# Performance work log

Measured on AMD Instinct MI355X. Metric: run time of the kernel, lower is better.

## Reference

```python
import jax, jax.numpy as jnp
import numpy as np

N_NODES = 50000
N_EDGES = 800000
N_FEAT = 256
HIDDEN = 128
N_CLASSES = 40


def gcn_conv(x, src, dst, W, b, n_nodes):
    """PyG GCNConv: add self-loops, symmetric normalization, x@W then scatter-add."""
    h = x @ W  # [N, out]
    loop = jnp.arange(n_nodes, dtype=src.dtype)
    s = jnp.concatenate([src, loop])  # [E+N]
    d = jnp.concatenate([dst, loop])
    deg = jax.ops.segment_sum(jnp.ones_like(d, dtype=h.dtype), d, num_segments=n_nodes)
    dinv = jnp.where(deg > 0, jax.lax.rsqrt(deg), 0.0)
    norm = dinv[s] * dinv[d]  # [E+N]
    msg = h[s] * norm[:, None]  # gather + scale
    out = jax.ops.segment_sum(msg, d, num_segments=n_nodes)  # scatter-add to targets
    return out + b


def setup_inputs() -> dict:
    key = jax.random.key(0)
    k1, k2, k3, k4 = jax.random.split(key, 4)
    x = jax.random.normal(k1, (N_NODES, N_FEAT), dtype=jnp.float32)
    edge_index = jax.random.randint(k2, (2, N_EDGES), 0, N_NODES, dtype=jnp.int32)
    # Glorot-style init for conv weights, zero bias (PyG default)
    W1 = jax.random.normal(k3, (N_FEAT, HIDDEN), dtype=jnp.float32) * (1.0 / np.sqrt(N_FEAT))
    b1 = jnp.zeros((HIDDEN,), dtype=jnp.float32)
    W2 = jax.random.normal(k4, (HIDDEN, N_CLASSES), dtype=jnp.float32) * (1.0 / np.sqrt(HIDDEN))
    b2 = jnp.zeros((N_CLASSES,), dtype=jnp.float32)
    return {"x": x, "edge_index": edge_index, "W1": W1, "b1": b1, "W2": W2, "b2": b2}


def reference(x, edge_index, W1, b1, W2, b2):
    # eval mode: dropout is identity
    src, dst = edge_index[0], edge_index[1]
    h = gcn_conv(x, src, dst, W1, b1, N_NODES)
    h = jax.nn.relu(h)
    h = gcn_conv(h, src, dst, W2, b2, N_NODES)
    return jax.nn.log_softmax(h, axis=1)
```

## Files before the change

### kernel.cpp

```cpp
#include <hip/hip_runtime.h>
#include <cstdint>

#define N_NODES 50000
#define N_EDGES 800000
#define N_FEAT 256
#define HIDDEN 128
#define N_CLASSES 40
#define NBUCKET 196
#define EPB 3125
#define BCAP 8192
#define ROWS_PAD 50048
#define H2S 64

typedef __attribute__((ext_vector_type(8))) short bf16x8;
typedef __attribute__((ext_vector_type(4))) float f32x4;

__device__ inline ushort f2bf(float f) {
    union { float f; uint u; } v; v.f = f;
    uint u = v.u;
    u += 0x7fff + ((u >> 16) & 1);
    return (ushort)(u >> 16);
}
__device__ inline float bflo(uint u) {
    union { uint u; float f; } v; v.u = u << 16; return v.f;
}
__device__ inline float bfhi(uint u) {
    union { uint u; float f; } v; v.u = u & 0xffff0000u; return v.f;
}


__global__ __launch_bounds__(256) void partition_repack(
        const int* __restrict__ src, const int* __restrict__ dst,
        int* __restrict__ cursor, uint* __restrict__ ebuf,
        const float* __restrict__ W1, ushort* __restrict__ Bp1) {
    __shared__ int h[NBUCKET];
    __shared__ int base[NBUCKET];
    __shared__ int cur[NBUCKET];
    int blk = blockIdx.x, t = threadIdx.x;
    int gid = blk * 256 + t;
    if (gid < 32768) {
        int j = gid & 7, lane = (gid >> 3) & 63, kt = (gid >> 9) & 7, nt = gid >> 12;
        int k = kt * 32 + (lane >> 4) * 8 + j;
        int n = nt * 16 + (lane & 15);
        Bp1[gid] = f2bf(W1[k * HIDDEN + n]);
    }
    if (t < NBUCKET) { h[t] = 0; cur[t] = 0; }
    __syncthreads();
    int eb = blk * EPB;
    for (int i = t; i < EPB; i += 256)
        atomicAdd(&h[dst[eb + i] >> 8], 1);
    __syncthreads();
    if (t < NBUCKET)
        base[t] = (h[t] > 0) ? atomicAdd(&cursor[t], h[t]) : 0;
    __syncthreads();
    for (int i = t; i < EPB; i += 256) {
        int d = dst[eb + i], sv = src[eb + i];
        int bk = d >> 8;
        int p = base[bk] + atomicAdd(&cur[bk], 1);
        ebuf[bk * BCAP + p] = ((uint)d << 16) | (uint)sv;
    }
}


__global__ __launch_bounds__(256) void bucket_csr(
        const uint* __restrict__ ebuf, const int* __restrict__ cursor,
        int* __restrict__ deg, float* __restrict__ dinv,
        int* __restrict__ rowptr, int* __restrict__ esrc) {
    __shared__ int s[256];
    __shared__ int cnt[256];
    __shared__ int exc[256];
    __shared__ int cur[256];
    int b = blockIdx.x, t = threadIdx.x;
    s[t] = (t < NBUCKET) ? cursor[t] : 0;
    __syncthreads();
    for (int off = 1; off < 256; off <<= 1) {
        int t2 = 0;
        if (t >= off) t2 = s[t - off];
        __syncthreads();
        s[t] += t2;
        __syncthreads();
    }
    int beg = (b > 0) ? s[b - 1] : 0;
    int ecnt = s[b] - beg;
    __syncthreads();
    cnt[t] = 0;
    cur[t] = 0;
    __syncthreads();
    const uint* eb = ebuf + (size_t)b * BCAP;
    for (int i = t; i < ecnt; i += 256)
        atomicAdd(&cnt[(eb[i] >> 16) & 255], 1);
    __syncthreads();
    int d = cnt[t];
    s[t] = d;
    __syncthreads();
    for (int off = 1; off < 256; off <<= 1) {
        int t2 = 0;
        if (t >= off) t2 = s[t - off];
        __syncthreads();
        s[t] += t2;
        __syncthreads();
    }
    exc[t] = s[t] - d;
    int node = b * 256 + t;
    if (node < N_NODES) {
        deg[node] = d;
        dinv[node] = rsqrtf((float)(d + 1));
        rowptr[node] = beg + exc[t];
    }
    __syncthreads();
    for (int i = t; i < ecnt; i += 256) {
        uint u = eb[i];
        int dl = (int)(u >> 16) & 255;
        int pos = beg + exc[dl] + atomicAdd(&cur[dl], 1);
        esrc[pos] = (int)(u & 0xffffu);
    }
}


#define XS_STRIDE 264

__global__ __launch_bounds__(256) void gemm1_mfma(const float* __restrict__ x,
                                                  const ushort* __restrict__ Bp,
                                                  ushort* __restrict__ h1b) {
    __shared__ ushort xs[64 * XS_STRIDE];
    int t = threadIdx.x;
    int row0 = blockIdx.x * 64;
#pragma unroll
    for (int i = 0; i < 16; ++i) {
        int idx = t + i * 256;
        int r = idx >> 6, kg = idx & 63;
        int row = row0 + r;
        float4 v = make_float4(0.f, 0.f, 0.f, 0.f);
        if (row < N_NODES) v = *(const float4*)(x + (size_t)row * N_FEAT + kg * 4);
        ushort4 u;
        u.x = f2bf(v.x); u.y = f2bf(v.y); u.z = f2bf(v.z); u.w = f2bf(v.w);
        *(ushort4*)(&xs[r * XS_STRIDE + kg * 4]) = u;
    }
    __syncthreads();
    int lane = t & 63, w = t >> 6;
    int r = lane & 15, q = lane >> 4;
    f32x4 acc[8] = {};
    for (int kt = 0; kt < 8; ++kt) {
        bf16x8 a = *(const bf16x8*)(&xs[(w * 16 + r) * XS_STRIDE + kt * 32 + q * 8]);
#pragma unroll
        for (int nt = 0; nt < 8; ++nt) {
            bf16x8 b = *(const bf16x8*)(Bp + (((nt * 8 + kt) * 64) + lane) * 8);
            acc[nt] = __builtin_amdgcn_mfma_f32_16x16x32_bf16(a, b, acc[nt], 0, 0, 0);
        }
    }
#pragma unroll
    for (int nt = 0; nt < 8; ++nt) {
        int col = nt * 16 + r;
#pragma unroll
        for (int reg = 0; reg < 4; ++reg) {
            int row = row0 + w * 16 + q * 4 + reg;
            if (row < N_NODES) h1b[(size_t)row * HIDDEN + col] = f2bf(acc[nt][reg]);
        }
    }
}


__global__ __launch_bounds__(256) void agg1_g(
        const int* __restrict__ rowptr, const int* __restrict__ deg,
        const int* __restrict__ esrc, const float* __restrict__ dinv,
        const ushort* __restrict__ h1b, const float* __restrict__ b1,
        ushort* __restrict__ hagb) {
    int w = threadIdx.x >> 6, lane = threadIdx.x & 63;
    int v = blockIdx.x * 4 + w;
    int q = lane >> 4, l = lane & 15;
    int beg = rowptr[v], d = deg[v];
    float dv = dinv[v];
    float a0 = 0.f, a1 = 0.f, a2 = 0.f, a3 = 0.f;
    float a4 = 0.f, a5 = 0.f, a6 = 0.f, a7 = 0.f;
    if (q == 0) {
        uint4 hv = *(const uint4*)(h1b + (size_t)v * HIDDEN + l * 8);
        float dd = dv * dv;
        a0 = bflo(hv.x) * dd; a1 = bfhi(hv.x) * dd;
        a2 = bflo(hv.y) * dd; a3 = bfhi(hv.y) * dd;
        a4 = bflo(hv.z) * dd; a5 = bfhi(hv.z) * dd;
        a6 = bflo(hv.w) * dd; a7 = bfhi(hv.w) * dd;
    }
    int e_l = (lane < d) ? esrc[beg + lane] : 0;
    float w_l = (lane < d) ? dinv[e_l] : 0.f;
    int dm = min(d, 64);
    int i = 0;
    for (; i + 8 <= dm; i += 8) {
        int s0 = __shfl(e_l, i + q, 64);
        int s1 = __shfl(e_l, i + 4 + q, 64);
        float g0 = __shfl(w_l, i + q, 64) * dv;
        float g1 = __shfl(w_l, i + 4 + q, 64) * dv;
        uint4 h0 = *(const uint4*)(h1b + (size_t)s0 * HIDDEN + l * 8);
        uint4 h1 = *(const uint4*)(h1b + (size_t)s1 * HIDDEN + l * 8);
        a0 = fmaf(bflo(h0.x), g0, a0); a1 = fmaf(bfhi(h0.x), g0, a1);
        a2 = fmaf(bflo(h0.y), g0, a2); a3 = fmaf(bfhi(h0.y), g0, a3);
        a4 = fmaf(bflo(h0.z), g0, a4); a5 = fmaf(bfhi(h0.z), g0, a5);
        a6 = fmaf(bflo(h0.w), g0, a6); a7 = fmaf(bfhi(h0.w), g0, a7);
        a0 = fmaf(bflo(h1.x), g1, a0); a1 = fmaf(bfhi(h1.x), g1, a1);
        a2 = fmaf(bflo(h1.y), g1, a2); a3 = fmaf(bfhi(h1.y), g1, a3);
        a4 = fmaf(bflo(h1.z), g1, a4); a5 = fmaf(bfhi(h1.z), g1, a5);
        a6 = fmaf(bflo(h1.w), g1, a6); a7 = fmaf(bfhi(h1.w), g1, a7);
    }
    for (; i < dm; i += 4) {
        int idx = i + q;
        int cl = idx & 63;
        int s0 = __shfl(e_l, cl, 64);
        float g0 = __shfl(w_l, cl, 64) * dv;
        if (idx >= dm) g0 = 0.f;
        uint4 h0 = *(const uint4*)(h1b + (size_t)s0 * HIDDEN + l * 8);
        a0 = fmaf(bflo(h0.x), g0, a0); a1 = fmaf(bfhi(h0.x), g0, a1);
        a2 = fmaf(bflo(h0.y), g0, a2); a3 = fmaf(bfhi(h0.y), g0, a3);
        a4 = fmaf(bflo(h0.z), g0, a4); a5 = fmaf(bfhi(h0.z), g0, a5);
        a6 = fmaf(bflo(h0.w), g0, a6); a7 = fmaf(bfhi(h0.w), g0, a7);
    }
    for (int j = 64 + q; j < d; j += 4) {
        int s = esrc[beg + j];
        float g = dinv[s] * dv;
        uint4 hs = *(const uint4*)(h1b + (size_t)s * HIDDEN + l * 8);
        a0 = fmaf(bflo(hs.x), g, a0); a1 = fmaf(bfhi(hs.x), g, a1);
        a2 = fmaf(bflo(hs.y), g, a2); a3 = fmaf(bfhi(hs.y), g, a3);
        a4 = fmaf(bflo(hs.z), g, a4); a5 = fmaf(bfhi(hs.z), g, a5);
        a6 = fmaf(bflo(hs.w), g, a6); a7 = fmaf(bfhi(hs.w), g, a7);
    }
    a0 += __shfl_xor(a0, 16, 64); a0 += __shfl_xor(a0, 32, 64);
    a1 += __shfl_xor(a1, 16, 64); a1 += __shfl_xor(a1, 32, 64);
    a2 += __shfl_xor(a2, 16, 64); a2 += __shfl_xor(a2, 32, 64);
    a3 += __shfl_xor(a3, 16, 64); a3 += __shfl_xor(a3, 32, 64);
    a4 += __shfl_xor(a4, 16, 64); a4 += __shfl_xor(a4, 32, 64);
    a5 += __shfl_xor(a5, 16, 64); a5 += __shfl_xor(a5, 32, 64);
    a6 += __shfl_xor(a6, 16, 64); a6 += __shfl_xor(a6, 32, 64);
    a7 += __shfl_xor(a7, 16, 64); a7 += __shfl_xor(a7, 32, 64);
    if (q == 0) {
        float4 bb0 = ((const float4*)b1)[l * 2];
        float4 bb1 = ((const float4*)b1)[l * 2 + 1];
        a0 += bb0.x; a1 += bb0.y; a2 += bb0.z; a3 += bb0.w;
        a4 += bb1.x; a5 += bb1.y; a6 += bb1.z; a7 += bb1.w;
        a0 = a0 > 0.f ? a0 : 0.f;  a1 = a1 > 0.f ? a1 : 0.f;
        a2 = a2 > 0.f ? a2 : 0.f;  a3 = a3 > 0.f ? a3 : 0.f;
        a4 = a4 > 0.f ? a4 : 0.f;  a5 = a5 > 0.f ? a5 : 0.f;
        a6 = a6 > 0.f ? a6 : 0.f;  a7 = a7 > 0.f ? a7 : 0.f;
        uint4 o;
        o.x = ((uint)f2bf(a1) << 16) | (uint)f2bf(a0);
        o.y = ((uint)f2bf(a3) << 16) | (uint)f2bf(a2);
        o.z = ((uint)f2bf(a5) << 16) | (uint)f2bf(a4);
        o.w = ((uint)f2bf(a7) << 16) | (uint)f2bf(a6);
        *(uint4*)(hagb + (size_t)v * HIDDEN + l * 8) = o;
    }
}


__global__ void repack_W2(const float* __restrict__ W, ushort* __restrict__ Bp) {
    int idx = blockIdx.x * 256 + threadIdx.x;
    if (idx >= 6144) return;
    int j = idx & 7, lane = (idx >> 3) & 63, kt = (idx >> 9) & 3, nt = idx >> 11;
    int k = kt * 32 + (lane >> 4) * 8 + j;
    int n = nt * 16 + (lane & 15);
    Bp[idx] = (n < N_CLASSES) ? f2bf(W[k * N_CLASSES + n]) : (ushort)0;
}

__global__ __launch_bounds__(256) void gemm2_mfma(const ushort* __restrict__ hagb,
                                                  const ushort* __restrict__ Bp,
                                                  ushort* __restrict__ h2b) {
    int t = threadIdx.x;
    int lane = t & 63, w = t >> 6;
    int r = lane & 15, q = lane >> 4;
    int row0 = blockIdx.x * 64;
    int arow = row0 + w * 16 + r;
    f32x4 acc[3] = {};
    for (int kt = 0; kt < 4; ++kt) {
        bf16x8 a = *(const bf16x8*)(hagb + (size_t)arow * HIDDEN + kt * 32 + q * 8);
#pragma unroll
        for (int nt = 0; nt < 3; ++nt) {
            bf16x8 b = *(const bf16x8*)(Bp + (((nt * 4 + kt) * 64) + lane) * 8);
            acc[nt] = __builtin_amdgcn_mfma_f32_16x16x32_bf16(a, b, acc[nt], 0, 0, 0);
        }
    }
#pragma unroll
    for (int nt = 0; nt < 3; ++nt) {
        int col = nt * 16 + r;
        if (col >= N_CLASSES) continue;
#pragma unroll
        for (int reg = 0; reg < 4; ++reg) {
            int row = row0 + w * 16 + q * 4 + reg;
            if (row < N_NODES) h2b[(size_t)row * H2S + col] = f2bf(acc[nt][reg]);
        }
    }
}


__global__ __launch_bounds__(256) void agg2_lsm(
        const int* __restrict__ rowptr, const int* __restrict__ deg,
        const int* __restrict__ esrc, const float* __restrict__ dinv,
        const ushort* __restrict__ h2b, const float* __restrict__ b2,
        float* __restrict__ out) {
    int w = threadIdx.x >> 6, lane = threadIdx.x & 63;
    int v = blockIdx.x * 4 + w;
    int g3 = lane / 20;
    int l = lane - g3 * 20;
    bool act = g3 < 3;
    int beg = rowptr[v], d = deg[v];
    float dv = dinv[v];
    float ax = 0.f, ay = 0.f;
    if (lane < 20) {
        uint hv = *(const uint*)(h2b + (size_t)v * H2S + l * 2);
        ax = bflo(hv) * dv * dv;
        ay = bfhi(hv) * dv * dv;
    }
    int e_l = (lane < d) ? esrc[beg + lane] : 0;
    float w_l = (lane < d) ? dinv[e_l] : 0.f;
    int dm = min(d, 64);
    int i = 0;
    for (; i + 6 <= dm; i += 6) {
        int s0 = __shfl(e_l, (i + g3) & 63, 64);
        int s1 = __shfl(e_l, (i + 3 + g3) & 63, 64);
        float g0 = __shfl(w_l, (i + g3) & 63, 64) * dv;
        float g1 = __shfl(w_l, (i + 3 + g3) & 63, 64) * dv;
        if (!act) { g0 = 0.f; g1 = 0.f; }
        uint h0 = *(const uint*)(h2b + (size_t)s0 * H2S + l * 2);
        uint h1 = *(const uint*)(h2b + (size_t)s1 * H2S + l * 2);
        ax = fmaf(bflo(h0), g0, ax); ay = fmaf(bfhi(h0), g0, ay);
        ax = fmaf(bflo(h1), g1, ax); ay = fmaf(bfhi(h1), g1, ay);
    }
    for (; i < dm; i += 3) {
        int idx = i + g3;
        int s0 = __shfl(e_l, idx & 63, 64);
        float g0 = __shfl(w_l, idx & 63, 64) * dv;
        if (!act || idx >= dm) g0 = 0.f;
        uint h0 = *(const uint*)(h2b + (size_t)s0 * H2S + l * 2);
        ax = fmaf(bflo(h0), g0, ax); ay = fmaf(bfhi(h0), g0, ay);
    }
    for (int j = 64 + g3; j < d; j += 3) {
        if (act) {
            int s = esrc[beg + j];
            float g = dinv[s] * dv;
            uint hs = *(const uint*)(h2b + (size_t)s * H2S + l * 2);
            ax = fmaf(bflo(hs), g, ax);
            ay = fmaf(bfhi(hs), g, ay);
        }
    }
    float fx1 = __shfl(ax, (lane + 20) & 63, 64);
    float fy1 = __shfl(ay, (lane + 20) & 63, 64);
    float fx2 = __shfl(ax, (lane + 40) & 63, 64);
    float fy2 = __shfl(ay, (lane + 40) & 63, 64);
    if (lane < 20) {
        ax += fx1 + fx2;
        ay += fy1 + fy2;
        float2 bb = ((const float2*)b2)[l];
        ax += bb.x; ay += bb.y;
    }
    float m = (lane < 20) ? fmaxf(ax, ay) : -INFINITY;
#pragma unroll
    for (int off = 32; off; off >>= 1) m = fmaxf(m, __shfl_xor(m, off, 64));
    float e = (lane < 20) ? (expf(ax - m) + expf(ay - m)) : 0.f;
#pragma unroll
    for (int off = 32; off; off >>= 1) e += __shfl_xor(e, off, 64);
    float ls = logf(e);
    if (lane < 20) {
        float2 o;
        o.x = ax - m - ls;
        o.y = ay - m - ls;
        ((float2*)(out + (size_t)v * N_CLASSES))[l] = o;
    }
}


extern "C" void kernel_launch(void* const* d_in, const int* in_sizes, int n_in,
                              void* d_out, int out_size, void* d_ws, size_t ws_size,
                              hipStream_t stream) {
    const float* x  = (const float*)d_in[0];
    const int*   ei = (const int*)d_in[1];
    const float* W1 = (const float*)d_in[2];
    const float* b1 = (const float*)d_in[3];
    const float* W2 = (const float*)d_in[4];
    const float* b2 = (const float*)d_in[5];
    const int* src = ei;
    const int* dst = ei + N_EDGES;
    float* out = (float*)d_out;

    char* ws = (char*)d_ws;
    size_t off = 0;
    auto alloc = [&](size_t bytes) {
        void* p = ws + off;
        off += (bytes + 255) & ~(size_t)255;
        return p;
    };
    int*    cursor = (int*)alloc((size_t)NBUCKET * 4);
    int*    deg    = (int*)alloc((size_t)N_NODES * 4);
    float*  dinv   = (float*)alloc((size_t)N_NODES * 4);
    int*    rowptr = (int*)alloc((size_t)N_NODES * 4);
    uint*   ebuf   = (uint*)alloc((size_t)NBUCKET * BCAP * 4);
    int*    esrc   = (int*)alloc((size_t)N_EDGES * 4);
    ushort* Bp1    = (ushort*)alloc((size_t)32768 * 2);
    ushort* Bp2    = (ushort*)alloc((size_t)6144 * 2);
    ushort* h1b    = (ushort*)alloc((size_t)ROWS_PAD * HIDDEN * 2);
    ushort* hagb   = (ushort*)alloc((size_t)ROWS_PAD * HIDDEN * 2);
    ushort* h2b    = (ushort*)alloc((size_t)ROWS_PAD * H2S * 2);

    hipMemsetAsync(cursor, 0, (size_t)NBUCKET * 4, stream);
    partition_repack<<<256, 256, 0, stream>>>(src, dst, cursor, ebuf, W1, Bp1);
    bucket_csr<<<NBUCKET, 256, 0, stream>>>(ebuf, cursor, deg, dinv, rowptr, esrc);

    repack_W2<<<24, 256, 0, stream>>>(W2, Bp2);
    gemm1_mfma<<<ROWS_PAD / 64, 256, 0, stream>>>(x, Bp1, h1b);
    agg1_g<<<N_NODES / 4, 256, 0, stream>>>(rowptr, deg, esrc, dinv, h1b, b1, hagb);
    gemm2_mfma<<<ROWS_PAD / 64, 256, 0, stream>>>(hagb, Bp2, h2b);
    agg2_lsm<<<N_NODES / 4, 256, 0, stream>>>(rowptr, deg, esrc, dinv, h2b, b2, out);
}
```

Before: 208.3 us.

## Switch intermediates to fp16 with packed half2 accumulation and remap agg2 lanes

Intermediate activations and weights move from bf16 to fp16, and the GEMMs now use the f16 MFMA. Both aggregation kernels accumulate with packed __hfma2 in half precision instead of unpacking to fp32 FMAs, which cuts ALU work per gathered row. agg2 is remapped to handle two nodes per wavefront with 32 lanes each, instead of one node with 60 active lanes. The W2 repack and the cursor memset are merged into one setup kernel, saving a launch. Accumulating sums in fp16 risks overflow and precision loss on high-degree nodes.

```diff
diff --git a/kernel.cpp b/kernel.cpp
--- a/kernel.cpp
+++ b/kernel.cpp
@@ -1,4 +1,5 @@
 #include <hip/hip_runtime.h>
+#include <hip/hip_fp16.h>
 #include <cstdint>
 
 #define N_NODES 50000
@@ -12,20 +13,29 @@
 #define ROWS_PAD 50048
 #define H2S 64
 
-typedef __attribute__((ext_vector_type(8))) short bf16x8;
+typedef _Float16 half8 __attribute__((ext_vector_type(8)));
 typedef __attribute__((ext_vector_type(4))) float f32x4;
 
-__device__ inline ushort f2bf(float f) {
-    union { float f; uint u; } v; v.f = f;
-    uint u = v.u;
-    u += 0x7fff + ((u >> 16) & 1);
-    return (ushort)(u >> 16);
-}
-__device__ inline float bflo(uint u) {
-    union { uint u; float f; } v; v.u = u << 16; return v.f;
-}
-__device__ inline float bfhi(uint u) {
-    union { uint u; float f; } v; v.u = u & 0xffff0000u; return v.f;
+__device__ inline ushort f2h(float f) {
+    return __half_as_ushort(__float2half_rn(f));
+}
+__device__ inline __half2 u2h2(uint u) {
+    union { uint u; __half2 h; } v; v.u = u; return v.h;
+}
+
+
+__global__ void setup_k(const float* __restrict__ W2, ushort* __restrict__ Bp2,
+                        int* __restrict__ cursor) {
+    int blk = blockIdx.x, t = threadIdx.x;
+    if (blk < 24) {
+        int idx = blk * 256 + t;
+        int j = idx & 7, lane = (idx >> 3) & 63, kt = (idx >> 9) & 3, nt = idx >> 11;
+        int k = kt * 32 + (lane >> 4) * 8 + j;
+        int n = nt * 16 + (lane & 15);
+        Bp2[idx] = (n < N_CLASSES) ? f2h(W2[k * N_CLASSES + n]) : (ushort)0;
+    } else {
+        if (t < NBUCKET) cursor[t] = 0;
+    }
 }
 
 
@@ -42,7 +52,7 @@
         int j = gid & 7, lane = (gid >> 3) & 63, kt = (gid >> 9) & 7, nt = gid >> 12;
         int k = kt * 32 + (lane >> 4) * 8 + j;
         int n = nt * 16 + (lane & 15);
-        Bp1[gid] = f2bf(W1[k * HIDDEN + n]);
+        Bp1[gid] = f2h(W1[k * HIDDEN + n]);
     }
     if (t < NBUCKET) { h[t] = 0; cur[t] = 0; }
     __syncthreads();
@@ -121,7 +131,7 @@
 
 __global__ __launch_bounds__(256) void gemm1_mfma(const float* __restrict__ x,
                                                   const ushort* __restrict__ Bp,
-                                                  ushort* __restrict__ h1b) {
+                                                  ushort* __restrict__ h1h) {
     __shared__ ushort xs[64 * XS_STRIDE];
     int t = threadIdx.x;
     int row0 = blockIdx.x * 64;
@@ -133,7 +143,7 @@
         float4 v = make_float4(0.f, 0.f, 0.f, 0.f);
         if (row < N_NODES) v = *(const float4*)(x + (size_t)row * N_FEAT + kg * 4);
         ushort4 u;
-        u.x = f2bf(v.x); u.y = f2bf(v.y); u.z = f2bf(v.z); u.w = f2bf(v.w);
+        u.x = f2h(v.x); u.y = f2h(v.y); u.z = f2h(v.z); u.w = f2h(v.w);
         *(ushort4*)(&xs[r * XS_STRIDE + kg * 4]) = u;
     }
     __syncthreads();
@@ -141,11 +151,11 @@
     int r = lane & 15, q = lane >> 4;
     f32x4 acc[8] = {};
     for (int kt = 0; kt < 8; ++kt) {
-        bf16x8 a = *(const bf16x8*)(&xs[(w * 16 + r) * XS_STRIDE + kt * 32 + q * 8]);
+        half8 a = *(const half8*)(&xs[(w * 16 + r) * XS_STRIDE + kt * 32 + q * 8]);
 #pragma unroll
         for (int nt = 0; nt < 8; ++nt) {
-            bf16x8 b = *(const bf16x8*)(Bp + (((nt * 8 + kt) * 64) + lane) * 8);
-            acc[nt] = __builtin_amdgcn_mfma_f32_16x16x32_bf16(a, b, acc[nt], 0, 0, 0);
+            half8 b = *(const half8*)(Bp + (((nt * 8 + kt) * 64) + lane) * 8);
+            acc[nt] = __builtin_amdgcn_mfma_f32_16x16x32_f16(a, b, acc[nt], 0, 0, 0);
         }
     }
 #pragma unroll
@@ -154,7 +164,7 @@
 #pragma unroll
         for (int reg = 0; reg < 4; ++reg) {
             int row = row0 + w * 16 + q * 4 + reg;
-            if (row < N_NODES) h1b[(size_t)row * HIDDEN + col] = f2bf(acc[nt][reg]);
+            if (row < N_NODES) h1h[(size_t)row * HIDDEN + col] = f2h(acc[nt][reg]);
         }
     }
 }
@@ -163,22 +173,23 @@
 __global__ __launch_bounds__(256) void agg1_g(
         const int* __restrict__ rowptr, const int* __restrict__ deg,
         const int* __restrict__ esrc, const float* __restrict__ dinv,
-        const ushort* __restrict__ h1b, const float* __restrict__ b1,
-        ushort* __restrict__ hagb) {
+        const ushort* __restrict__ h1h, const float* __restrict__ b1,
+        ushort* __restrict__ hagh) {
     int w = threadIdx.x >> 6, lane = threadIdx.x & 63;
     int v = blockIdx.x * 4 + w;
     int q = lane >> 4, l = lane & 15;
     int beg = rowptr[v], d = deg[v];
     float dv = dinv[v];
-    float a0 = 0.f, a1 = 0.f, a2 = 0.f, a3 = 0.f;
-    float a4 = 0.f, a5 = 0.f, a6 = 0.f, a7 = 0.f;
+    __half2 z = __float2half2_rn(0.f);
+    __half2 c0 = z, c1 = z, c2 = z, c3 = z;
+    __half2 e0 = z, e1 = z, e2 = z, e3 = z;
     if (q == 0) {
-        uint4 hv = *(const uint4*)(h1b + (size_t)v * HIDDEN + l * 8);
-        float dd = dv * dv;
-        a0 = bflo(hv.x) * dd; a1 = bfhi(hv.x) * dd;
-        a2 = bflo(hv.y) * dd; a3 = bfhi(hv.y) * dd;
-        a4 = bflo(hv.z) * dd; a5 = bfhi(hv.z) * dd;
-        a6 = bflo(hv.w) * dd; a7 = bfhi(hv.w) * dd;
+        uint4 hv = *(const uint4*)(h1h + (size_t)v * HIDDEN + l * 8);
+        __half2 gs = __float2half2_rn(dv * dv);
+        c0 = __hfma2(u2h2(hv.x), gs, c0);
+        c1 = __hfma2(u2h2(hv.y), gs, c1);
+        c2 = __hfma2(u2h2(hv.z), gs, c2);
+        c3 = __hfma2(u2h2(hv.w), gs, c3);
     }
     int e_l = (lane < d) ? esrc[beg + lane] : 0;
     float w_l = (lane < d) ? dinv[e_l] : 0.f;
@@ -189,16 +200,18 @@
         int s1 = __shfl(e_l, i + 4 + q, 64);
         float g0 = __shfl(w_l, i + q, 64) * dv;
         float g1 = __shfl(w_l, i + 4 + q, 64) * dv;
-        uint4 h0 = *(const uint4*)(h1b + (size_t)s0 * HIDDEN + l * 8);
-        uint4 h1 = *(const uint4*)(h1b + (size_t)s1 * HIDDEN + l * 8);
-        a0 = fmaf(bflo(h0.x), g0, a0); a1 = fmaf(bfhi(h0.x), g0, a1);
-        a2 = fmaf(bflo(h0.y), g0, a2); a3 = fmaf(bfhi(h0.y), g0, a3);
-        a4 = fmaf(bflo(h0.z), g0, a4); a5 = fmaf(bfhi(h0.z), g0, a5);
-        a6 = fmaf(bflo(h0.w), g0, a6); a7 = fmaf(bfhi(h0.w), g0, a7);
-        a0 = fmaf(bflo(h1.x), g1, a0); a1 = fmaf(bfhi(h1.x), g1, a1);
-        a2 = fmaf(bflo(h1.y), g1, a2); a3 = fmaf(bfhi(h1.y), g1, a3);
-        a4 = fmaf(bflo(h1.z), g1, a4); a5 = fmaf(bfhi(h1.z), g1, a5);
-        a6 = fmaf(bflo(h1.w), g1, a6); a7 = fmaf(bfhi(h1.w), g1, a7);
+        __half2 gh0 = __float2half2_rn(g0);
+        __half2 gh1 = __float2half2_rn(g1);
+        uint4 h0 = *(const uint4*)(h1h + (size_t)s0 * HIDDEN + l * 8);
+        uint4 h1 = *(const uint4*)(h1h + (size_t)s1 * HIDDEN + l * 8);
+        c0 = __hfma2(u2h2(h0.x), gh0, c0);
+        c1 = __hfma2(u2h2(h0.y), gh0, c1);
+        c2 = __hfma2(u2h2(h0.z), gh0, c2);
+        c3 = __hfma2(u2h2(h0.w), gh0, c3);
+        e0 = __hfma2(u2h2(h1.x), gh1, e0);
+        e1 = __hfma2(u2h2(h1.y), gh1, e1);
+        e2 = __hfma2(u2h2(h1.z), gh1, e2);
+        e3 = __hfma2(u2h2(h1.w), gh1, e3);
     }
     for (; i < dm; i += 4) {
         int idx = i + q;
@@ -206,21 +219,30 @@
         int s0 = __shfl(e_l, cl, 64);
         float g0 = __shfl(w_l, cl, 64) * dv;
         if (idx >= dm) g0 = 0.f;
-        uint4 h0 = *(const uint4*)(h1b + (size_t)s0 * HIDDEN + l * 8);
-        a0 = fmaf(bflo(h0.x), g0, a0); a1 = fmaf(bfhi(h0.x), g0, a1);
-        a2 = fmaf(bflo(h0.y), g0, a2); a3 = fmaf(bfhi(h0.y), g0, a3);
-        a4 = fmaf(bflo(h0.z), g0, a4); a5 = fmaf(bfhi(h0.z), g0, a5);
-        a6 = fmaf(bflo(h0.w), g0, a6); a7 = fmaf(bfhi(h0.w), g0, a7);
+        __half2 gh0 = __float2half2_rn(g0);
+        uint4 h0 = *(const uint4*)(h1h + (size_t)s0 * HIDDEN + l * 8);
+        c0 = __hfma2(u2h2(h0.x), gh0, c0);
+        c1 = __hfma2(u2h2(h0.y), gh0, c1);
+        c2 = __hfma2(u2h2(h0.z), gh0, c2);
+        c3 = __hfma2(u2h2(h0.w), gh0, c3);
     }
     for (int j = 64 + q; j < d; j += 4) {
         int s = esrc[beg + j];
-        float g = dinv[s] * dv;
-        uint4 hs = *(const uint4*)(h1b + (size_t)s * HIDDEN + l * 8);
-        a0 = fmaf(bflo(hs.x), g, a0); a1 = fmaf(bfhi(hs.x), g, a1);
-        a2 = fmaf(bflo(hs.y), g, a2); a3 = fmaf(bfhi(hs.y), g, a3);
-        a4 = fmaf(bflo(hs.z), g, a4); a5 = fmaf(bfhi(hs.z), g, a5);
-        a6 = fmaf(bflo(hs.w), g, a6); a7 = fmaf(bfhi(hs.w), g, a7);
-    }
+        __half2 g = __float2half2_rn(dinv[s] * dv);
+        uint4 hs = *(const uint4*)(h1h + (size_t)s * HIDDEN + l * 8);
+        c0 = __hfma2(u2h2(hs.x), g, c0);
+        c1 = __hfma2(u2h2(hs.y), g, c1);
+        c2 = __hfma2(u2h2(hs.z), g, c2);
+        c3 = __hfma2(u2h2(hs.w), g, c3);
+    }
+    float2 f0 = __half22float2(c0), f1 = __half22float2(c1);
+    float2 f2 = __half22float2(c2), f3 = __half22float2(c3);
+    float2 g0 = __half22float2(e0), g1 = __half22float2(e1);
+    float2 g2 = __half22float2(e2), g3 = __half22float2(e3);
+    float a0 = f0.x + g0.x, a1 = f0.y + g0.y;
+    float a2 = f1.x + g1.x, a3 = f1.y + g1.y;
+    float a4 = f2.x + g2.x, a5 = f2.y + g2.y;
+    float a6 = f3.x + g3.x, a7 = f3.y + g3.y;
     a0 += __shfl_xor(a0, 16, 64); a0 += __shfl_xor(a0, 32, 64);
     a1 += __shfl_xor(a1, 16, 64); a1 += __shfl_xor(a1, 32, 64);
     a2 += __shfl_xor(a2, 16, 64); a2 += __shfl_xor(a2, 32, 64);
@@ -238,28 +260,21 @@
         a2 = a2 > 0.f ? a2 : 0.f;  a3 = a3 > 0.f ? a3 : 0.f;
         a4 = a4 > 0.f ? a4 : 0.f;  a5 = a5 > 0.f ? a5 : 0.f;
         a6 = a6 > 0.f ? a6 : 0.f;  a7 = a7 > 0.f ? a7 : 0.f;
-        uint4 o;
-        o.x = ((uint)f2bf(a1) << 16) | (uint)f2bf(a0);
-        o.y = ((uint)f2bf(a3) << 16) | (uint)f2bf(a2);
-        o.z = ((uint)f2bf(a5) << 16) | (uint)f2bf(a4);
-        o.w = ((uint)f2bf(a7) << 16) | (uint)f2bf(a6);
-        *(uint4*)(hagb + (size_t)v * HIDDEN + l * 8) = o;
-    }
-}
-
-
-__global__ void repack_W2(const float* __restrict__ W, ushort* __restrict__ Bp) {
-    int idx = blockIdx.x * 256 + threadIdx.x;
-    if (idx >= 6144) return;
-    int j = idx & 7, lane = (idx >> 3) & 63, kt = (idx >> 9) & 3, nt = idx >> 11;
-    int k = kt * 32 + (lane >> 4) * 8 + j;
-    int n = nt * 16 + (lane & 15);
-    Bp[idx] = (n < N_CLASSES) ? f2bf(W[k * N_CLASSES + n]) : (ushort)0;
-}
-
-__global__ __launch_bounds__(256) void gemm2_mfma(const ushort* __restrict__ hagb,
+        ushort4 o;
+        o.x = f2h(a0);
+        uint4 ov;
+        ov.x = ((uint)f2h(a1) << 16) | (uint)f2h(a0);
+        ov.y = ((uint)f2h(a3) << 16) | (uint)f2h(a2);
+        ov.z = ((uint)f2h(a5) << 16) | (uint)f2h(a4);
+        ov.w = ((uint)f2h(a7) << 16) | (uint)f2h(a6);
+        *(uint4*)(hagh + (size_t)v * HIDDEN + l * 8) = ov;
+    }
+}
+
+
+__global__ __launch_bounds__(256) void gemm2_mfma(const ushort* __restrict__ hagh,
                                                   const ushort* __restrict__ Bp,
-                                                  ushort* __restrict__ h2b) {
+                                                  ushort* __restrict__ h2h) {
     int t = threadIdx.x;
     int lane = t & 63, w = t >> 6;
     int r = lane & 15, q = lane >> 4;
@@ -267,11 +282,11 @@
     int arow = row0 + w * 16 + r;
     f32x4 acc[3] = {};
     for (int kt = 0; kt < 4; ++kt) {
-        bf16x8 a = *(const bf16x8*)(hagb + (size_t)arow * HIDDEN + kt * 32 + q * 8);
+        half8 a = *(const half8*)(hagh + (size_t)arow * HIDDEN + kt * 32 + q * 8);
 #pragma unroll
         for (int nt = 0; nt < 3; ++nt) {
-            bf16x8 b = *(const bf16x8*)(Bp + (((nt * 4 + kt) * 64) + lane) * 8);
-            acc[nt] = __builtin_amdgcn_mfma_f32_16x16x32_bf16(a, b, acc[nt], 0, 0, 0);
+            half8 b = *(const half8*)(Bp + (((nt * 4 + kt) * 64) + lane) * 8);
+            acc[nt] = __builtin_amdgcn_mfma_f32_16x16x32_f16(a, b, acc[nt], 0, 0, 0);
         }
     }
 #pragma unroll
@@ -281,7 +296,7 @@
 #pragma unroll
         for (int reg = 0; reg < 4; ++reg) {
             int row = row0 + w * 16 + q * 4 + reg;
-            if (row < N_NODES) h2b[(size_t)row * H2S + col] = f2bf(acc[nt][reg]);
+            if (row < N_NODES) h2h[(size_t)row * H2S + col] = f2h(acc[nt][reg]);
         }
     }
 }
@@ -290,71 +305,70 @@
 __global__ __launch_bounds__(256) void agg2_lsm(
         const int* __restrict__ rowptr, const int* __restrict__ deg,
         const int* __restrict__ esrc, const float* __restrict__ dinv,
-        const ushort* __restrict__ h2b, const float* __restrict__ b2,
+        const ushort* __restrict__ h2h, const float* __restrict__ b2,
         float* __restrict__ out) {
-    int w = threadIdx.x >> 6, lane = threadIdx.x & 63;
-    int v = blockIdx.x * 4 + w;
-    int g3 = lane / 20;
-    int l = lane - g3 * 20;
-    bool act = g3 < 3;
+    int t = threadIdx.x;
+    int w = t >> 6, lane = t & 63;
+    int half = lane >> 5, l = lane & 31;
+    int v = blockIdx.x * 8 + w * 2 + half;
     int beg = rowptr[v], d = deg[v];
     float dv = dinv[v];
-    float ax = 0.f, ay = 0.f;
-    if (lane < 20) {
-        uint hv = *(const uint*)(h2b + (size_t)v * H2S + l * 2);
-        ax = bflo(hv) * dv * dv;
-        ay = bfhi(hv) * dv * dv;
-    }
-    int e_l = (lane < d) ? esrc[beg + lane] : 0;
-    float w_l = (lane < d) ? dinv[e_l] : 0.f;
-    int dm = min(d, 64);
+    __half2 z = __float2half2_rn(0.f);
+    __half2 cA = z, cB = z;
+    {
+        uint hv = *(const uint*)(h2h + (size_t)v * H2S + (l & 31) * 2);
+        cA = __hfma2(u2h2(hv), __float2half2_rn(dv * dv), cA);
+    }
+    int e_l = (l < d) ? esrc[beg + l] : 0;
+    float w_l = (l < d) ? dinv[e_l] : 0.f;
+    int dm = min(d, 32);
+    int base = half * 32;
     int i = 0;
-    for (; i + 6 <= dm; i += 6) {
-        int s0 = __shfl(e_l, (i + g3) & 63, 64);
-        int s1 = __shfl(e_l, (i + 3 + g3) & 63, 64);
-        float g0 = __shfl(w_l, (i + g3) & 63, 64) * dv;
-        float g1 = __shfl(w_l, (i + 3 + g3) & 63, 64) * dv;
-        if (!act) { g0 = 0.f; g1 = 0.f; }
-        uint h0 = *(const uint*)(h2b + (size_t)s0 * H2S + l * 2);
-        uint h1 = *(const uint*)(h2b + (size_t)s1 * H2S + l * 2);
-        ax = fmaf(bflo(h0), g0, ax); ay = fmaf(bfhi(h0), g0, ay);
-        ax = fmaf(bflo(h1), g1, ax); ay = fmaf(bfhi(h1), g1, ay);
-    }
-    for (; i < dm; i += 3) {
-        int idx = i + g3;
-        int s0 = __shfl(e_l, idx & 63, 64);
-        float g0 = __shfl(w_l, idx & 63, 64) * dv;
-        if (!act || idx >= dm) g0 = 0.f;
-        uint h0 = *(const uint*)(h2b + (size_t)s0 * H2S + l * 2);
-        ax = fmaf(bflo(h0), g0, ax); ay = fmaf(bfhi(h0), g0, ay);
-    }
-    for (int j = 64 + g3; j < d; j += 3) {
-        if (act) {
-            int s = esrc[beg + j];
-            float g = dinv[s] * dv;
-            uint hs = *(const uint*)(h2b + (size_t)s * H2S + l * 2);
-            ax = fmaf(bflo(hs), g, ax);
-            ay = fmaf(bfhi(hs), g, ay);
-        }
-    }
-    float fx1 = __shfl(ax, (lane + 20) & 63, 64);
-    float fy1 = __shfl(ay, (lane + 20) & 63, 64);
-    float fx2 = __shfl(ax, (lane + 40) & 63, 64);
-    float fy2 = __shfl(ay, (lane + 40) & 63, 64);
-    if (lane < 20) {
-        ax += fx1 + fx2;
-        ay += fy1 + fy2;
+    for (; i + 4 <= dm; i += 4) {
+        int s0 = __shfl(e_l, base + i + 0, 64);
+        int s1 = __shfl(e_l, base + i + 1, 64);
+        int s2 = __shfl(e_l, base + i + 2, 64);
+        int s3 = __shfl(e_l, base + i + 3, 64);
+        float g0 = __shfl(w_l, base + i + 0, 64) * dv;
+        float g1 = __shfl(w_l, base + i + 1, 64) * dv;
+        float g2 = __shfl(w_l, base + i + 2, 64) * dv;
+        float g3 = __shfl(w_l, base + i + 3, 64) * dv;
+        uint h0 = *(const uint*)(h2h + (size_t)s0 * H2S + l * 2);
+        uint h1 = *(const uint*)(h2h + (size_t)s1 * H2S + l * 2);
+        uint h2 = *(const uint*)(h2h + (size_t)s2 * H2S + l * 2);
+        uint h3 = *(const uint*)(h2h + (size_t)s3 * H2S + l * 2);
+        cA = __hfma2(u2h2(h0), __float2half2_rn(g0), cA);
+        cB = __hfma2(u2h2(h1), __float2half2_rn(g1), cB);
+        cA = __hfma2(u2h2(h2), __float2half2_rn(g2), cA);
+        cB = __hfma2(u2h2(h3), __float2half2_rn(g3), cB);
+    }
+    for (; i < dm; ++i) {
+        int s0 = __shfl(e_l, base + i, 64);
+        float g0 = __shfl(w_l, base + i, 64) * dv;
+        uint h0 = *(const uint*)(h2h + (size_t)s0 * H2S + l * 2);
+        cA = __hfma2(u2h2(h0), __float2half2_rn(g0), cA);
+    }
+    for (i = 32; i < d; ++i) {
+        int s = esrc[beg + i];
+        float g = dinv[s] * dv;
+        uint hs = *(const uint*)(h2h + (size_t)s * H2S + l * 2);
+        cA = __hfma2(u2h2(hs), __float2half2_rn(g), cA);
+    }
+    float2 fA = __half22float2(cA);
+    float2 fB = __half22float2(cB);
+    float ax = fA.x + fB.x, ay = fA.y + fB.y;
+    if (l < 20) {
         float2 bb = ((const float2*)b2)[l];
         ax += bb.x; ay += bb.y;
     }
-    float m = (lane < 20) ? fmaxf(ax, ay) : -INFINITY;
-#pragma unroll
-    for (int off = 32; off; off >>= 1) m = fmaxf(m, __shfl_xor(m, off, 64));
-    float e = (lane < 20) ? (expf(ax - m) + expf(ay - m)) : 0.f;
-#pragma unroll
-    for (int off = 32; off; off >>= 1) e += __shfl_xor(e, off, 64);
+    float m = (l < 20) ? fmaxf(ax, ay) : -INFINITY;
+#pragma unroll
+    for (int off = 16; off; off >>= 1) m = fmaxf(m, __shfl_xor(m, off, 64));
+    float e = (l < 20) ? (expf(ax - m) + expf(ay - m)) : 0.f;
+#pragma unroll
+    for (int off = 16; off; off >>= 1) e += __shfl_xor(e, off, 64);
     float ls = logf(e);
-    if (lane < 20) {
+    if (l < 20) {
         float2 o;
         o.x = ax - m - ls;
         o.y = ay - m - ls;
@@ -391,17 +405,16 @@
     int*    esrc   = (int*)alloc((size_t)N_EDGES * 4);
     ushort* Bp1    = (ushort*)alloc((size_t)32768 * 2);
     ushort* Bp2    = (ushort*)alloc((size_t)6144 * 2);
-    ushort* h1b    = (ushort*)alloc((size_t)ROWS_PAD * HIDDEN * 2);
-    ushort* hagb   = (ushort*)alloc((size_t)ROWS_PAD * HIDDEN * 2);
-    ushort* h2b    = (ushort*)alloc((size_t)ROWS_PAD * H2S * 2);
-
-    hipMemsetAsync(cursor, 0, (size_t)NBUCKET * 4, stream);
+    ushort* h1h    = (ushort*)alloc((size_t)ROWS_PAD * HIDDEN * 2);
+    ushort* hagh   = (ushort*)alloc((size_t)ROWS_PAD * HIDDEN * 2);
+    ushort* h2h    = (ushort*)alloc((size_t)ROWS_PAD * H2S * 2);
+
+    setup_k<<<25, 256, 0, stream>>>(W2, Bp2, cursor);
     partition_repack<<<256, 256, 0, stream>>>(src, dst, cursor, ebuf, W1, Bp1);
     bucket_csr<<<NBUCKET, 256, 0, stream>>>(ebuf, cursor, deg, dinv, rowptr, esrc);
 
-    repack_W2<<<24, 256, 0, stream>>>(W2, Bp2);
-    gemm1_mfma<<<ROWS_PAD / 64, 256, 0, stream>>>(x, Bp1, h1b);
-    agg1_g<<<N_NODES / 4, 256, 0, stream>>>(rowptr, deg, esrc, dinv, h1b, b1, hagb);
-    gemm2_mfma<<<ROWS_PAD / 64, 256, 0, stream>>>(hagb, Bp2, h2b);
-    agg2_lsm<<<N_NODES / 4, 256, 0, stream>>>(rowptr, deg, esrc, dinv, h2b, b2, out);
-}
+    gemm1_mfma<<<ROWS_PAD / 64, 256, 0, stream>>>(x, Bp1, h1h);
+    agg1_g<<<N_NODES / 4, 256, 0, stream>>>(rowptr, deg, esrc, dinv, h1h, b1, hagh);
+    gemm2_mfma<<<ROWS_PAD / 64, 256, 0, stream>>>(hagh, Bp2, h2h);
+    agg2_lsm<<<N_NODES / 8, 256, 0, stream>>>(rowptr, deg, esrc, dinv, h2h, b2, out);
+}
```

Measured after the change: 199.0 us. -4.5%, faster.
